# Performance work log

Hardware: AMD Instinct MI355X
Metric: run time of the kernel (lower is better)

Reference implementation:

```python
import jax, jax.numpy as jnp
import numpy as np

H = 1024      # hidden_dim == memory_dim (required by seq-axis concat)
M = 1024      # memory_dim
FF = 4096     # ff_dim
WIN = 16      # window_size
SLOTS = 10    # persistent memory slots
B, S = 2, 4096
EPS_LN = 1e-5
EPS_NORM = 1e-12


def _layernorm(x, g, b):
    m = jnp.mean(x, axis=-1, keepdims=True)
    v = jnp.var(x, axis=-1, keepdims=True)
    return (x - m) / jnp.sqrt(v + EPS_LN) * g + b


def setup_inputs() -> dict:
    key = jax.random.key(0)
    ks = jax.random.split(key, 12)

    def lin_w(k, out_d, in_d):
        return jax.random.normal(k, (out_d, in_d), jnp.float32) / np.sqrt(in_d)

    return {
        "x": jax.random.normal(ks[0], (B, S, H), jnp.float32),
        "mem_W": lin_w(ks[1], M, M), "mem_b": jnp.zeros((M,), jnp.float32),
        "P": jax.random.normal(ks[2], (SLOTS, M), jnp.float32),
        "Wi": lin_w(ks[3], M, H), "bi": jnp.zeros((M,), jnp.float32),
        "Wl1": lin_w(ks[4], M, M), "bl1": jnp.zeros((M,), jnp.float32),
        "Wl2": lin_w(ks[5], M, M), "bl2": jnp.zeros((M,), jnp.float32),
        "Wo": lin_w(ks[6], H, M), "bo": jnp.zeros((H,), jnp.float32),
        "fgate": jnp.ones((1,), jnp.float32),
        "lrate": jnp.ones((1,), jnp.float32),
        "Wg": lin_w(ks[7], H, 2 * H), "bg": jnp.zeros((H,), jnp.float32),
        "W1": lin_w(ks[8], FF, H), "b1": jnp.zeros((FF,), jnp.float32),
        "W2": lin_w(ks[9], H, FF), "b2": jnp.zeros((H,), jnp.float32),
        "g1": jnp.ones((H,), jnp.float32), "be1": jnp.zeros((H,), jnp.float32),
        "g2": jnp.ones((H,), jnp.float32), "be2": jnp.zeros((H,), jnp.float32),
        "g3": jnp.ones((H,), jnp.float32), "be3": jnp.zeros((H,), jnp.float32),
    }


def reference(x, mem_W, mem_b, P, Wi, bi, Wl1, bl1, Wl2, bl2, Wo, bo,
              fgate, lrate, Wg, bg, W1, b1, W2, b2,
              g1, be1, g2, be2, g3, be3):
    b, s, h = x.shape
    # k = concat(x, persistent) along seq; v = k.clone()
    k_full = jnp.concatenate([x, jnp.broadcast_to(P, (b,) + P.shape)], axis=1)  # [B, S+SLOTS, H]

    # sit at positions >= S and are never inside the window, so only x is attended.
    idx = jnp.arange(s)[:, None] + jnp.arange(-WIN, 1)[None, :]
    valid = idx >= 0
    k_win = k_full[:, jnp.maximum(idx, 0)]
    scores = jnp.einsum('bsh,bswh->bsw', x, k_win) * (h ** -0.5)
    scores = jnp.where(valid[None], scores, -jnp.inf)
    attn_out = jnp.einsum('bsw,bswh->bsh', jax.nn.softmax(scores, axis=-1), k_win)
    x1 = _layernorm(x + attn_out, g1, be1)

    # --- neural long-term memory (key == value since v = k.clone())
    kv = k_full.reshape(-1, h)
    kn = kv / jnp.maximum(jnp.linalg.norm(kv, axis=-1, keepdims=True), EPS_NORM)
    kp = kn @ Wi.T + bi          # projected key; value_proj is identical
    vp = kp
    hdd = jax.nn.silu(kp @ Wl1.T + bl1)
    hdd = jax.nn.silu(hdd @ Wl2.T + bl2)
    pred = hdd @ mem_W.T + mem_b
    diff = pred - vp
    n, m = diff.shape
    grad_W = (2.0 / (n * m)) * diff.T @ hdd          # d mse / d mem_W
    W_new = (1.0 - fgate) * mem_W + lrate * grad_W   # test-time memory update
    mem_out = hdd @ W_new.T + mem_b
    mo = (mem_out @ Wo.T + bo).reshape(b, -1, h)[:, :s]  # align with x seq length

    # --- gated fusion + FFN
    gate = jax.nn.sigmoid(jnp.concatenate([x1, mo], axis=-1) @ Wg.T + bg)
    combined = gate * x1 + (1.0 - gate) * mo
    x2 = _layernorm(x1 + combined, g2, be2)
    ff = jax.nn.silu(x2 @ W1.T + b1) @ W2.T + b2
    return _layernorm(x2 + ff, g3, be3)
```

## Files before the change

### kernel.cpp

```cpp
#include <hip/hip_runtime.h>
#include <hip/hip_bf16.h>

#define WIN 16
#define SLOTS 10
#define SS 4096
#define NTOK 8192
#define NKV 8212
#define NPOS 4106
#define NATTB 2048
#define NKVB 2053

typedef unsigned short u16;
typedef unsigned int u32;
typedef __attribute__((ext_vector_type(8))) short short8;
typedef __attribute__((ext_vector_type(4))) float f32x4;

__device__ __forceinline__ u16 f2bf(float f){
  union { float f; u32 u; } a; a.f = f;
  u32 r = (a.u + 0x7fff + ((a.u >> 16) & 1)) >> 16;
  return (u16)r;
}
__device__ __forceinline__ float bf2f(u16 v){
  union { u32 u; float f; } a; a.u = ((u32)v) << 16;
  return a.f;
}
__device__ __forceinline__ float wred(float v){
  #pragma unroll
  for (int off=32; off; off>>=1) v += __shfl_xor(v, off, 64);
  return v;
}

#define GLOAD(gp, lp) __builtin_amdgcn_global_load_lds( \
    (const __attribute__((address_space(1))) void*)(gp), \
    (__attribute__((address_space(3))) void*)(lp), 16, 0, 0)

#define FENCE_BARRIER() do { \
    __builtin_amdgcn_sched_barrier(0); \
    __builtin_amdgcn_s_barrier(); \
    __builtin_amdgcn_sched_barrier(0); \
  } while(0)

__global__ __launch_bounds__(256) void cvt_all(
    const float4* __restrict__ s0, const float4* __restrict__ s1,
    const float4* __restrict__ s2, const float4* __restrict__ s3,
    const float4* __restrict__ s4, const float4* __restrict__ s5,
    const float4* __restrict__ s6, const float4* __restrict__ s7,
    ushort4* __restrict__ d0, ushort4* __restrict__ d1,
    ushort4* __restrict__ d2, ushort4* __restrict__ d3,
    ushort4* __restrict__ d4, ushort4* __restrict__ d5,
    ushort4* __restrict__ d6, ushort4* __restrict__ d7)
{
  int i = blockIdx.x * 256 + threadIdx.x;
  const float4* s; ushort4* d; int base;
  if      (i <  262144){ s=s0; d=d0; base=0; }
  else if (i <  524288){ s=s1; d=d1; base=262144; }
  else if (i <  786432){ s=s2; d=d2; base=524288; }
  else if (i < 1048576){ s=s3; d=d3; base=786432; }
  else if (i < 1310720){ s=s4; d=d4; base=1048576; }
  else if (i < 1835008){ s=s5; d=d5; base=1310720; }
  else if (i < 2883584){ s=s6; d=d6; base=1835008; }
  else                 { s=s7; d=d7; base=2883584; }
  float4 v = s[i - base];
  ushort4 o; o.x=f2bf(v.x); o.y=f2bf(v.y); o.z=f2bf(v.z); o.w=f2bf(v.w);
  d[i - base] = o;
}

__global__ __launch_bounds__(256) void attn_kv(
    const float* __restrict__ x, const float* __restrict__ P,
    const float* __restrict__ g1, const float* __restrict__ be1,
    u16* __restrict__ x1b, u16* __restrict__ kn)
{
  const int blk = blockIdx.x;
  const int t = threadIdx.x, lane = t & 63, wid = t >> 6;
  if (blk >= NATTB){
    const int r = (blk - NATTB)*4 + wid;
    if (r >= NKV) return;
    const int b = r / NPOS;
    const int pos = r - b*NPOS;
    const float4* src = (const float4*)((pos < SS) ? (x + (((size_t)b*SS + pos) << 10))
                                                   : (P + ((size_t)(pos - SS) << 10)));
    float4 v[4];
    float ss = 0.f;
    #pragma unroll
    for (int e=0;e<4;e++){
      v[e] = src[(lane<<2)+e];
      ss += v[e].x*v[e].x + v[e].y*v[e].y + v[e].z*v[e].z + v[e].w*v[e].w;
    }
    ss = wred(ss);
    float inv = 1.f / fmaxf(sqrtf(ss), 1e-12f);
    ushort4* dst = (ushort4*)kn + ((size_t)r << 8);
    #pragma unroll
    for (int e=0;e<4;e++){
      ushort4 o; o.x=f2bf(v[e].x*inv); o.y=f2bf(v[e].y*inv); o.z=f2bf(v[e].z*inv); o.w=f2bf(v[e].w*inv);
      dst[(lane<<2)+e] = o;
    }
    return;
  }
  const int n = blk*4 + wid;
  const int b = n >> 12, s = n & 4095;
  const float* xb = x + ((size_t)b << 22);
  const float4* qp = (const float4*)(xb + ((size_t)s << 10));
  float4 q[4];
  #pragma unroll
  for (int e=0;e<4;e++) q[e] = qp[(lane<<2)+e];

  const int j0 = (s >= WIN) ? 0 : (WIN - s);
  float m = -3.0e38f, l = 0.f;
  float4 o[4];
  #pragma unroll
  for (int e=0;e<4;e++) o[e] = make_float4(0.f,0.f,0.f,0.f);

  for (int j = j0; j < 17; ++j){
    const float4* kp_ = (const float4*)(xb + ((size_t)(s - WIN + j) << 10));
    float4 kk[4];
    float dp = 0.f;
    #pragma unroll
    for (int e=0;e<4;e++){
      kk[e] = kp_[(lane<<2)+e];
      dp += q[e].x*kk[e].x + q[e].y*kk[e].y + q[e].z*kk[e].z + q[e].w*kk[e].w;
    }
    dp = wred(dp) * 0.03125f;
    float mn = fmaxf(m, dp);
    float sc = __expf(m - mn);
    float e_ = __expf(dp - mn);
    l = l*sc + e_;
    #pragma unroll
    for (int e=0;e<4;e++){
      o[e].x = o[e].x*sc + e_*kk[e].x;
      o[e].y = o[e].y*sc + e_*kk[e].y;
      o[e].z = o[e].z*sc + e_*kk[e].z;
      o[e].w = o[e].w*sc + e_*kk[e].w;
    }
    m = mn;
  }
  const float il = 1.f / l;
  float s1 = 0.f, s2 = 0.f;
  float4 y[4];
  #pragma unroll
  for (int e=0;e<4;e++){
    y[e].x = q[e].x + o[e].x*il;
    y[e].y = q[e].y + o[e].y*il;
    y[e].z = q[e].z + o[e].z*il;
    y[e].w = q[e].w + o[e].w*il;
    s1 += y[e].x + y[e].y + y[e].z + y[e].w;
    s2 += y[e].x*y[e].x + y[e].y*y[e].y + y[e].z*y[e].z + y[e].w*y[e].w;
  }
  s1 = wred(s1); s2 = wred(s2);
  float mean = s1 * (1.f/1024.f);
  float var  = s2 * (1.f/1024.f) - mean*mean;
  float rstd = 1.f/sqrtf(var + 1e-5f);
  ushort4* dst = (ushort4*)x1b + ((size_t)n << 8);
  #pragma unroll
  for (int e=0;e<4;e++){
    float4 gv = ((const float4*)g1)[(lane<<2)+e];
    float4 bv = ((const float4*)be1)[(lane<<2)+e];
    ushort4 ob;
    ob.x = f2bf((y[e].x-mean)*rstd*gv.x + bv.x);
    ob.y = f2bf((y[e].y-mean)*rstd*gv.y + bv.y);
    ob.z = f2bf((y[e].z-mean)*rstd*gv.z + bv.z);
    ob.w = f2bf((y[e].w-mean)*rstd*gv.w + bv.w);
    dst[(lane<<2)+e] = ob;
  }
}

template<int EPI, int SPLITA>
__global__ __launch_bounds__(256) void gemm_nt(
    const u16* __restrict__ A, const u16* __restrict__ A2,
    const u16* __restrict__ Bmat, const float* __restrict__ bias,
    const u16* __restrict__ auxb,
    float* __restrict__ Cf, u16* __restrict__ Cb,
    int N, int O, int ldA, int ldB, int klen)
{
  __shared__ __align__(16) u16 lA[4][128*32];
  __shared__ __align__(16) u16 lB[4][128*32];
  const int t = threadIdx.x;
  const int lane = t & 63;
  const int bm0 = blockIdx.x * 128;
  const int bn0 = blockIdx.y * 128;
  const int wid = t >> 6;
  const int wr = wid >> 1, wc = wid & 1;
  const int nkh = klen >> 5;

  f32x4 acc[4][4];
  #pragma unroll
  for (int i=0;i<4;i++)
    #pragma unroll
    for (int j=0;j<4;j++)
      acc[i][j] = (f32x4){0.f,0.f,0.f,0.f};

  const int srow = t >> 2;
  const int sch  = t & 3;
  const int csw  = ((sch ^ ((srow >> 1) & 3)) << 3);

  int gr0 = bm0 + srow;      gr0 = gr0 < N ? gr0 : N-1;
  int gr1 = bm0 + srow + 64; gr1 = gr1 < N ? gr1 : N-1;
  int gb0 = bn0 + srow;      gb0 = gb0 < O ? gb0 : O-1;
  int gb1 = bn0 + srow + 64; gb1 = gb1 < O ? gb1 : O-1;
  const u16* bA0 = A + (size_t)gr0*(size_t)ldA + csw;
  const u16* bA1 = A + (size_t)gr1*(size_t)ldA + csw;
  const u16* bA20 = SPLITA ? (A2 + ((size_t)gr0 << 10) + csw) : nullptr;
  const u16* bA21 = SPLITA ? (A2 + ((size_t)gr1 << 10) + csw) : nullptr;
  const u16* bB0 = Bmat + (size_t)gb0*(size_t)ldB + csw;
  const u16* bB1 = Bmat + (size_t)gb1*(size_t)ldB + csw;
  const int dLo = t << 3;
  const int dHi = (t << 3) + 2048;

  auto stage = [&](int j){
    const int kb = j << 5;
    const int s = j & 3;
    const u16* a0 = SPLITA ? ((kb < 1024) ? bA0 + kb : bA20 + (kb - 1024)) : bA0 + kb;
    const u16* a1 = SPLITA ? ((kb < 1024) ? bA1 + kb : bA21 + (kb - 1024)) : bA1 + kb;
    GLOAD(a0, &lA[s][dLo]);
    GLOAD(a1, &lA[s][dHi]);
    GLOAD(bB0 + kb, &lB[s][dLo]);
    GLOAD(bB1 + kb, &lB[s][dHi]);
  };

  stage(0);
  if (nkh > 1) stage(1);
  if (nkh > 2) stage(2);

  const int l15 = lane & 15;
  const int cq  = lane >> 4;
  const int soff = ((cq ^ ((l15 >> 1) & 3)) << 3);

  for (int j = 0; j < nkh; ++j){
    const int s = j & 3;
    const int cnt = 4*((j+1 < nkh) + (j+2 < nkh));
    if (cnt == 8)      { asm volatile("s_waitcnt vmcnt(8)" ::: "memory"); }
    else if (cnt == 4) { asm volatile("s_waitcnt vmcnt(4)" ::: "memory"); }
    else               { asm volatile("s_waitcnt vmcnt(0)" ::: "memory"); }
    FENCE_BARRIER();
    short8 af[4], bfv[4];
    #pragma unroll
    for (int mi=0;mi<4;mi++)
      af[mi] = *(const short8*)(&lA[s][((wr*64 + mi*16 + l15) * 32) + soff]);
    #pragma unroll
    for (int ni=0;ni<4;ni++)
      bfv[ni] = *(const short8*)(&lB[s][((wc*64 + ni*16 + l15) * 32) + soff]);
    if (j + 3 < nkh) stage(j + 3);
    __builtin_amdgcn_sched_barrier(0);
    __builtin_amdgcn_s_setprio(1);
    #pragma unroll
    for (int mi=0;mi<4;mi++)
      #pragma unroll
      for (int ni=0;ni<4;ni++)
        acc[mi][ni] = __builtin_amdgcn_mfma_f32_16x16x32_bf16(af[mi], bfv[ni], acc[mi][ni], 0, 0, 0);
    __builtin_amdgcn_s_setprio(0);
    __builtin_amdgcn_sched_barrier(0);
  }

  const int rbase = (lane >> 4) * 4;
  const int cidx = lane & 15;
  #pragma unroll
  for (int mi=0;mi<4;mi++){
    #pragma unroll
    for (int r=0;r<4;r++){
      const int n = bm0 + wr*64 + mi*16 + rbase + r;
      if (n >= N) continue;
      #pragma unroll
      for (int ni=0;ni<4;ni++){
        const int o = bn0 + wc*64 + ni*16 + cidx;
        float v = acc[mi][ni][r] + bias[o];
        if (EPI == 6){
          int b = n / NPOS;
          int pos = n - b*NPOS;
          if (pos < SS){
            Cb[(((size_t)(b*SS + pos)) << 10) + o] = f2bf(v);
          }
        } else {
          size_t idx = (size_t)n*(size_t)O + o;
          if (EPI == 0){ Cf[idx] = v; }
          else if (EPI == 1){ float sv = v/(1.f+__expf(-v)); Cb[idx] = f2bf(sv); }
          else if (EPI == 2){ Cb[idx] = f2bf(v); }
          else if (EPI == 4){ Cb[idx] = f2bf(v - bf2f(auxb[idx])); }
          else if (EPI == 5){ Cb[idx] = f2bf(1.f/(1.f+__expf(-v))); }
        }
      }
    }
  }
}

template<int EPI>
__global__ __launch_bounds__(512, 2) void gemm_256(
    const u16* __restrict__ A, const u16* __restrict__ Bmat,
    const float* __restrict__ bias,
    float* __restrict__ Cf, float* __restrict__ Cf2, u16* __restrict__ Cb,
    int N, int O, int ldA, int ldB, int klen)
{
  __shared__ __align__(16) u16 lA[4][256*32];
  __shared__ __align__(16) u16 lB[4][256*32];
  const int t = threadIdx.x;
  const int lane = t & 63;
  const int wid = t >> 6;
  const int wr = wid >> 2, wc = wid & 3;
  const int bm0 = blockIdx.x * 256;
  const int bn0 = blockIdx.y * 256;
  const size_t koff = (size_t)blockIdx.z * (size_t)klen;
  const int nkh = klen >> 5;

  f32x4 acc[8][4];
  #pragma unroll
  for (int i=0;i<8;i++)
    #pragma unroll
    for (int j=0;j<4;j++)
      acc[i][j] = (f32x4){0.f,0.f,0.f,0.f};

  const int srow = t >> 2;
  const int sch  = t & 3;
  const int csw  = ((sch ^ ((srow >> 1) & 3)) << 3);
  int gr0 = bm0 + srow;       gr0 = gr0 < N ? gr0 : N-1;
  int gr1 = bm0 + srow + 128; gr1 = gr1 < N ? gr1 : N-1;
  int gb0 = bn0 + srow;       gb0 = gb0 < O ? gb0 : O-1;
  int gb1 = bn0 + srow + 128; gb1 = gb1 < O ? gb1 : O-1;
  const u16* baseA0 = A    + (size_t)gr0*(size_t)ldA + koff + csw;
  const u16* baseA1 = A    + (size_t)gr1*(size_t)ldA + koff + csw;
  const u16* baseB0 = Bmat + (size_t)gb0*(size_t)ldB + koff + csw;
  const u16* baseB1 = Bmat + (size_t)gb1*(size_t)ldB + koff + csw;
  const int ldsLo = srow*32 + (sch << 3);
  const int ldsHi = (srow + 128)*32 + (sch << 3);

  auto stageA = [&](int j){
    const int kb = j << 5;
    const int s = j & 3;
    GLOAD(baseA0 + kb, &lA[s][ldsLo]);
    GLOAD(baseA1 + kb, &lA[s][ldsHi]);
  };
  auto stageB = [&](int j){
    const int kb = j << 5;
    const int s = j & 3;
    GLOAD(baseB0 + kb, &lB[s][ldsLo]);
    GLOAD(baseB1 + kb, &lB[s][ldsHi]);
  };

  stageA(0); stageB(0);
  if (nkh > 1){ stageA(1); stageB(1); }
  if (nkh > 2){ stageA(2); stageB(2); }

  const int l15 = lane & 15;
  const int cq  = lane >> 4;
  const int chS = ((cq ^ ((l15 >> 1) & 3)) << 3);

  for (int j = 0; j < nkh; ++j){
    const int s = j & 3;
    const int rem = nkh - 1 - j;
    if (rem >= 2)      { asm volatile("s_waitcnt vmcnt(8)" ::: "memory"); }
    else if (rem == 1) { asm volatile("s_waitcnt vmcnt(4)" ::: "memory"); }
    else               { asm volatile("s_waitcnt vmcnt(0)" ::: "memory"); }
    FENCE_BARRIER();
    short8 af[4], bfv[4];
    #pragma unroll
    for (int ni=0;ni<4;ni++)
      bfv[ni] = *(const short8*)(&lB[s][((wc*64 + ni*16 + l15) * 32) + chS]);
    #pragma unroll
    for (int mi=0;mi<4;mi++)
      af[mi] = *(const short8*)(&lA[s][((wr*128 + mi*16 + l15) * 32) + chS]);
    if (j + 3 < nkh) stageA(j + 3);
    __builtin_amdgcn_sched_barrier(0);
    __builtin_amdgcn_s_setprio(1);
    #pragma unroll
    for (int mi=0;mi<4;mi++)
      #pragma unroll
      for (int ni=0;ni<4;ni++)
        acc[mi][ni] = __builtin_amdgcn_mfma_f32_16x16x32_bf16(af[mi], bfv[ni], acc[mi][ni], 0, 0, 0);
    __builtin_amdgcn_s_setprio(0);
    __builtin_amdgcn_sched_barrier(0);
    FENCE_BARRIER();
    #pragma unroll
    for (int mi=0;mi<4;mi++)
      af[mi] = *(const short8*)(&lA[s][((wr*128 + (mi+4)*16 + l15) * 32) + chS]);
    if (j + 3 < nkh) stageB(j + 3);
    __builtin_amdgcn_sched_barrier(0);
    __builtin_amdgcn_s_setprio(1);
    #pragma unroll
    for (int mi=0;mi<4;mi++)
      #pragma unroll
      for (int ni=0;ni<4;ni++)
        acc[mi+4][ni] = __builtin_amdgcn_mfma_f32_16x16x32_bf16(af[mi], bfv[ni], acc[mi+4][ni], 0, 0, 0);
    __builtin_amdgcn_s_setprio(0);
    __builtin_amdgcn_sched_barrier(0);
  }

  float* dstf = (EPI == 7) ? (blockIdx.z ? Cf2 : Cf) : Cf;
  const int rbase = (lane >> 4) * 4;
  const int cidx = lane & 15;
  #pragma unroll
  for (int mi=0;mi<8;mi++){
    #pragma unroll
    for (int r=0;r<4;r++){
      const int n = bm0 + wr*128 + mi*16 + rbase + r;
      if (n >= N) continue;
      #pragma unroll
      for (int ni=0;ni<4;ni++){
        const int o = bn0 + wc*64 + ni*16 + cidx;
        size_t idx = (size_t)n*(size_t)O + o;
        if (EPI == 7){ dstf[idx] = acc[mi][ni][r]; }
        else {
          float v = acc[mi][ni][r] + bias[o];
          if (EPI == 0){ Cf[idx] = v; }
          else if (EPI == 1){ float sv = v/(1.f+__expf(-v)); Cb[idx] = f2bf(sv); }
          else if (EPI == 2){ Cb[idx] = f2bf(v); }
        }
      }
    }
  }
}

#define NSPLIT 6
__global__ __launch_bounds__(256) void gemm_tn(
    const u16* __restrict__ A, const u16* __restrict__ B,
    float* __restrict__ part0, float* __restrict__ part1)
{
  __shared__ __align__(16) u16 lA[128*64];
  __shared__ __align__(16) u16 lB[128*64];
  const int t = threadIdx.x, lane = t & 63;
  const int i0 = blockIdx.x * 128, j0 = blockIdx.y * 128, z = blockIdx.z;
  const int wid = t >> 6, wr = wid >> 1, wc = wid & 1;
  const int TILES = (NKV + 63) >> 6;
  const int PER = (TILES + NSPLIT - 1) / NSPLIT;
  const int kt0 = z * PER;
  const int ktend = (kt0 + PER < TILES) ? (kt0 + PER) : TILES;

  f32x4 acc[4][4];
  #pragma unroll
  for (int i=0;i<4;i++)
    #pragma unroll
    for (int j=0;j<4;j++)
      acc[i][j] = (f32x4){0.f,0.f,0.f,0.f};

  const int p = t & 31;
  const int g = t >> 5;

  auto loadr = [&](int kt, short8 R[8]){
    const int n0 = kt << 6;
    const int na = n0 + 2*p, nb = na + 1;
    short8 z8 = (short8){0,0,0,0,0,0,0,0};
    R[0]=z8;R[1]=z8;R[2]=z8;R[3]=z8;R[4]=z8;R[5]=z8;R[6]=z8;R[7]=z8;
    if (na < NKV){
      const u16* ra = A + (size_t)na*1024 + i0 + g*16;
      R[0] = *(const short8*)ra; R[1] = *(const short8*)(ra+8);
      const u16* rb = B + (size_t)na*1024 + j0 + g*16;
      R[4] = *(const short8*)rb; R[5] = *(const short8*)(rb+8);
    }
    if (nb < NKV){
      const u16* ra = A + (size_t)nb*1024 + i0 + g*16;
      R[2] = *(const short8*)ra; R[3] = *(const short8*)(ra+8);
      const u16* rb = B + (size_t)nb*1024 + j0 + g*16;
      R[6] = *(const short8*)rb; R[7] = *(const short8*)(rb+8);
    }
  };

  short8 cr[8], nr[8];
  loadr(kt0, cr);

  const int pc = p >> 2, pl = p & 3;

  for (int kt = kt0; kt < ktend; ++kt){
    if (kt + 1 < ktend) loadr(kt + 1, nr);
    asm volatile("" ::: "memory");
    FENCE_BARRIER();
    u32* wA = (u32*)lA; u32* wB = (u32*)lB;
    #pragma unroll
    for (int e=0;e<8;e++){
      const int s = (pc ^ e) * 4 + pl;
      wA[(g*16 + e)*32 + s]     = ((u32)(u16)cr[0][e]) | (((u32)(u16)cr[2][e]) << 16);
      wB[(g*16 + e)*32 + s]     = ((u32)(u16)cr[4][e]) | (((u32)(u16)cr[6][e]) << 16);
    }
    #pragma unroll
    for (int e=0;e<8;e++){
      const int s = (pc ^ e) * 4 + pl;
      wA[(g*16 + 8 + e)*32 + s] = ((u32)(u16)cr[1][e]) | (((u32)(u16)cr[3][e]) << 16);
      wB[(g*16 + 8 + e)*32 + s] = ((u32)(u16)cr[5][e]) | (((u32)(u16)cr[7][e]) << 16);
    }
    asm volatile("s_waitcnt lgkmcnt(0)" ::: "memory");
    FENCE_BARRIER();
    const int l15 = lane & 15;
    const int rx = l15 & 7;
    const int cq = lane >> 4;
    #pragma unroll
    for (int kk=0;kk<2;kk++){
      const int soff = (((kk*4 + cq) ^ rx) << 3);
      short8 af[4], bfv[4];
      #pragma unroll
      for (int mi=0;mi<4;mi++)
        af[mi] = *(const short8*)(lA + ((wr*64 + mi*16 + l15) << 6) + soff);
      #pragma unroll
      for (int ni=0;ni<4;ni++)
        bfv[ni] = *(const short8*)(lB + ((wc*64 + ni*16 + l15) << 6) + soff);
      #pragma unroll
      for (int mi=0;mi<4;mi++)
        #pragma unroll
        for (int ni=0;ni<4;ni++)
          acc[mi][ni] = __builtin_amdgcn_mfma_f32_16x16x32_bf16(af[mi], bfv[ni], acc[mi][ni], 0, 0, 0);
    }
    #pragma unroll
    for (int e=0;e<8;e++) cr[e] = nr[e];
  }

  float* dst = (z < 4) ? (part0 + ((size_t)z << 20)) : (part1 + ((size_t)(z-4) << 20));
  const int rbase = (lane >> 4) * 4;
  const int cidx = lane & 15;
  #pragma unroll
  for (int mi=0;mi<4;mi++)
    #pragma unroll
    for (int r=0;r<4;r++){
      const int i = i0 + wr*64 + mi*16 + rbase + r;
      #pragma unroll
      for (int ni=0;ni<4;ni++){
        const int j = j0 + wc*64 + ni*16 + cidx;
        dst[((size_t)i << 10) + j] = acc[mi][ni][r];
      }
    }
}

__global__ __launch_bounds__(256) void wnew_k(const float* __restrict__ part0,
                                              const float* __restrict__ part1,
                                              const float* __restrict__ memW,
                                              const float* __restrict__ fg,
                                              const float* __restrict__ lr,
                                              u16* __restrict__ out)
{
  int i = blockIdx.x*256 + threadIdx.x;
  float s = part0[i] + part0[i + (1<<20)] + part0[i + (2<<20)] + part0[i + (3<<20)]
          + part1[i] + part1[i + (1<<20)];
  const float scale = 2.f / ((float)NKV * 1024.f);
  float v = (1.f - fg[0])*memW[i] + lr[0]*scale*s;
  out[i] = f2bf(v);
}

__global__ __launch_bounds__(256) void ln_gate(
    const u16* __restrict__ x1b, const u16* __restrict__ gateb,
    const u16* __restrict__ mob, const float* __restrict__ g2,
    const float* __restrict__ be2, u16* __restrict__ x2b)
{
  const int n = blockIdx.x;
  const int t = threadIdx.x, lane = t & 63, w = t >> 6;
  const size_t rb = (size_t)n << 8;
  ushort4 xa = ((const ushort4*)x1b)[rb+t];
  ushort4 ga = ((const ushort4*)gateb)[rb+t];
  ushort4 ma = ((const ushort4*)mob)[rb+t];
  float a0=bf2f(xa.x),a1=bf2f(xa.y),a2=bf2f(xa.z),a3=bf2f(xa.w);
  float g0=bf2f(ga.x),g1v=bf2f(ga.y),g2v=bf2f(ga.z),g3v=bf2f(ga.w);
  float m0=bf2f(ma.x),m1=bf2f(ma.y),m2=bf2f(ma.z),m3=bf2f(ma.w);
  float y0 = a0 + g0*a0 + (1.f-g0)*m0;
  float y1 = a1 + g1v*a1 + (1.f-g1v)*m1;
  float y2 = a2 + g2v*a2 + (1.f-g2v)*m2;
  float y3 = a3 + g3v*a3 + (1.f-g3v)*m3;
  float s1 = y0+y1+y2+y3;
  float s2 = y0*y0+y1*y1+y2*y2+y3*y3;
  #pragma unroll
  for (int off=32; off; off>>=1){ s1 += __shfl_xor(s1, off, 64); s2 += __shfl_xor(s2, off, 64); }
  __shared__ float rsh[8];
  if (lane == 0){ rsh[w] = s1; rsh[4+w] = s2; }
  __syncthreads();
  float S1 = rsh[0]+rsh[1]+rsh[2]+rsh[3];
  float S2 = rsh[4]+rsh[5]+rsh[6]+rsh[7];
  float mean = S1 * (1.f/1024.f);
  float var  = S2 * (1.f/1024.f) - mean*mean;
  float rstd = 1.f/sqrtf(var + 1e-5f);
  float4 gv = ((const float4*)g2)[t];
  float4 bv = ((const float4*)be2)[t];
  ushort4 ob;
  ob.x = f2bf((y0-mean)*rstd*gv.x + bv.x);
  ob.y = f2bf((y1-mean)*rstd*gv.y + bv.y);
  ob.z = f2bf((y2-mean)*rstd*gv.z + bv.z);
  ob.w = f2bf((y3-mean)*rstd*gv.w + bv.w);
  ((ushort4*)x2b)[rb + t] = ob;
}

__global__ __launch_bounds__(256) void ln_final(
    const u16* __restrict__ x2b, const float* __restrict__ g3,
    const float* __restrict__ be3, float* __restrict__ out)
{
  const int n = blockIdx.x;
  const int t = threadIdx.x, lane = t & 63, w = t >> 6;
  const size_t rb = (size_t)n << 8;
  ushort4 xa = ((const ushort4*)x2b)[rb+t];
  float4 f = ((const float4*)out)[rb+t];
  float y0 = bf2f(xa.x)+f.x, y1 = bf2f(xa.y)+f.y, y2 = bf2f(xa.z)+f.z, y3 = bf2f(xa.w)+f.w;
  float s1 = y0+y1+y2+y3;
  float s2 = y0*y0+y1*y1+y2*y2+y3*y3;
  #pragma unroll
  for (int off=32; off; off>>=1){ s1 += __shfl_xor(s1, off, 64); s2 += __shfl_xor(s2, off, 64); }
  __shared__ float rsh[8];
  if (lane == 0){ rsh[w] = s1; rsh[4+w] = s2; }
  __syncthreads();
  float S1 = rsh[0]+rsh[1]+rsh[2]+rsh[3];
  float S2 = rsh[4]+rsh[5]+rsh[6]+rsh[7];
  float mean = S1 * (1.f/1024.f);
  float var  = S2 * (1.f/1024.f) - mean*mean;
  float rstd = 1.f/sqrtf(var + 1e-5f);
  float4 gv = ((const float4*)g3)[t];
  float4 bv = ((const float4*)be3)[t];
  float4 o;
  o.x = (y0-mean)*rstd*gv.x + bv.x;
  o.y = (y1-mean)*rstd*gv.y + bv.y;
  o.z = (y2-mean)*rstd*gv.z + bv.z;
  o.w = (y3-mean)*rstd*gv.w + bv.w;
  ((float4*)out)[rb + t] = o;
}

__global__ __launch_bounds__(256) void ln_final2(
    const u16* __restrict__ x2b, const float* __restrict__ p0,
    const float* __restrict__ p1, const float* __restrict__ b2,
    const float* __restrict__ g3, const float* __restrict__ be3,
    float* __restrict__ out)
{
  const int n = blockIdx.x;
  const int t = threadIdx.x, lane = t & 63, w = t >> 6;
  const size_t rb = (size_t)n << 8;
  ushort4 xa = ((const ushort4*)x2b)[rb+t];
  float4 f0 = ((const float4*)p0)[rb+t];
  float4 f1 = ((const float4*)p1)[rb+t];
  float4 bb = ((const float4*)b2)[t];
  float y0 = bf2f(xa.x)+f0.x+f1.x+bb.x, y1 = bf2f(xa.y)+f0.y+f1.y+bb.y;
  float y2 = bf2f(xa.z)+f0.z+f1.z+bb.z, y3 = bf2f(xa.w)+f0.w+f1.w+bb.w;
  float s1 = y0+y1+y2+y3;
  float s2 = y0*y0+y1*y1+y2*y2+y3*y3;
  #pragma unroll
  for (int off=32; off; off>>=1){ s1 += __shfl_xor(s1, off, 64); s2 += __shfl_xor(s2, off, 64); }
  __shared__ float rsh[8];
  if (lane == 0){ rsh[w] = s1; rsh[4+w] = s2; }
  __syncthreads();
  float S1 = rsh[0]+rsh[1]+rsh[2]+rsh[3];
  float S2 = rsh[4]+rsh[5]+rsh[6]+rsh[7];
  float mean = S1 * (1.f/1024.f);
  float var  = S2 * (1.f/1024.f) - mean*mean;
  float rstd = 1.f/sqrtf(var + 1e-5f);
  float4 gv = ((const float4*)g3)[t];
  float4 bv = ((const float4*)be3)[t];
  float4 o;
  o.x = (y0-mean)*rstd*gv.x + bv.x;
  o.y = (y1-mean)*rstd*gv.y + bv.y;
  o.z = (y2-mean)*rstd*gv.z + bv.z;
  o.w = (y3-mean)*rstd*gv.w + bv.w;
  ((float4*)out)[rb + t] = o;
}

extern "C" void kernel_launch(void* const* d_in, const int* in_sizes, int n_in,
                              void* d_out, int out_size, void* d_ws, size_t ws_size,
                              hipStream_t stream)
{
  const float* x    = (const float*)d_in[0];
  const float* memW = (const float*)d_in[1];
  const float* memb = (const float*)d_in[2];
  const float* P    = (const float*)d_in[3];
  const float* Wi   = (const float*)d_in[4];
  const float* bi   = (const float*)d_in[5];
  const float* Wl1  = (const float*)d_in[6];
  const float* bl1  = (const float*)d_in[7];
  const float* Wl2  = (const float*)d_in[8];
  const float* bl2  = (const float*)d_in[9];
  const float* Wo   = (const float*)d_in[10];
  const float* bo   = (const float*)d_in[11];
  const float* fg   = (const float*)d_in[12];
  const float* lr   = (const float*)d_in[13];
  const float* Wg   = (const float*)d_in[14];
  const float* bg   = (const float*)d_in[15];
  const float* W1   = (const float*)d_in[16];
  const float* b1   = (const float*)d_in[17];
  const float* W2   = (const float*)d_in[18];
  const float* b2   = (const float*)d_in[19];
  const float* g1   = (const float*)d_in[20];
  const float* be1  = (const float*)d_in[21];
  const float* g2   = (const float*)d_in[22];
  const float* be2  = (const float*)d_in[23];
  const float* g3   = (const float*)d_in[24];
  const float* be3  = (const float*)d_in[25];
  float* out = (float*)d_out;

  const size_t SZ_TOK = (size_t)NTOK*1024*2;
  const size_t SZ_KV  = (size_t)NKV*1024*2;
  char* base = (char*)d_ws;
  size_t off = 0;
  auto alloc = [&](size_t bytes) -> char* {
    char* p = base + off;
    off += (bytes + 255) & ~(size_t)255;
    return p;
  };
  u16* x1b   = (u16*)alloc(SZ_TOK);
  u16* knb   = (u16*)alloc(SZ_KV);
  u16* h1b   = (u16*)alloc(SZ_KV);
  u16* hddb  = (u16*)alloc(SZ_KV);
  u16* kpb   = (u16*)alloc(SZ_KV);
  u16* wnewb = (u16*)alloc((size_t)1024*1024*2);
  u16* WiB   = (u16*)alloc((size_t)1024*1024*2);
  u16* Wl1B  = (u16*)alloc((size_t)1024*1024*2);
  u16* Wl2B  = (u16*)alloc((size_t)1024*1024*2);
  u16* memWB = (u16*)alloc((size_t)1024*1024*2);
  u16* WoB   = (u16*)alloc((size_t)1024*1024*2);
  u16* WgB   = (u16*)alloc((size_t)1024*2048*2);
  u16* W1B   = (u16*)alloc((size_t)4096*1024*2);
  u16* W2B   = (u16*)alloc((size_t)1024*4096*2);
  const size_t off_base = off;
  if (ws_size < off_base) return;

  float* ffp0 = (float*)alloc((size_t)NTOK*1024*4);
  float* ffp1 = (float*)alloc((size_t)NTOK*1024*4);
  const bool use_split_ff2 = (ws_size >= off);

  u16*   diffb   = knb;
  float* part0   = (float*)kpb;
  float* part1   = (float*)WiB;
  u16*   memoutb = knb;
  u16*   mob     = h1b;
  u16*   gateb   = hddb;
  u16*   x2b     = kpb;
  u16*   ff1b    = x1b;

  cvt_all<<<15360, 256, 0, stream>>>(
      (const float4*)Wi, (const float4*)Wl1, (const float4*)Wl2, (const float4*)memW,
      (const float4*)Wo, (const float4*)Wg, (const float4*)W1, (const float4*)W2,
      (ushort4*)WiB, (ushort4*)Wl1B, (ushort4*)Wl2B, (ushort4*)memWB,
      (ushort4*)WoB, (ushort4*)WgB, (ushort4*)W1B, (ushort4*)W2B);

  attn_kv<<<NATTB + NKVB, 256, 0, stream>>>(x, P, g1, be1, x1b, knb);

  dim3 gkv(65, 8, 1);
  gemm_nt<2,0><<<gkv, 256, 0, stream>>>(knb, nullptr, WiB, bi, nullptr, nullptr, kpb, NKV, 1024, 1024, 1024, 1024);
  gemm_nt<1,0><<<gkv, 256, 0, stream>>>(kpb, nullptr, Wl1B, bl1, nullptr, nullptr, h1b, NKV, 1024, 1024, 1024, 1024);
  gemm_nt<1,0><<<gkv, 256, 0, stream>>>(h1b, nullptr, Wl2B, bl2, nullptr, nullptr, hddb, NKV, 1024, 1024, 1024, 1024);
  gemm_nt<4,0><<<gkv, 256, 0, stream>>>(hddb, nullptr, memWB, memb, kpb, nullptr, diffb, NKV, 1024, 1024, 1024, 1024);
  gemm_tn<<<dim3(8, 8, NSPLIT), 256, 0, stream>>>(diffb, hddb, part0, part1);
  wnew_k<<<4096, 256, 0, stream>>>(part0, part1, memW, fg, lr, wnewb);
  gemm_nt<2,0><<<gkv, 256, 0, stream>>>(hddb, nullptr, wnewb, memb, nullptr, nullptr, memoutb, NKV, 1024, 1024, 1024, 1024);
  gemm_nt<6,0><<<gkv, 256, 0, stream>>>(memoutb, nullptr, WoB, bo, nullptr, nullptr, mob, NKV, 1024, 1024, 1024, 1024);
  gemm_nt<5,1><<<dim3(64, 8, 1), 256, 0, stream>>>(x1b, mob, WgB, bg, nullptr, nullptr, gateb, NTOK, 1024, 1024, 2048, 2048);
  ln_gate<<<NTOK, 256, 0, stream>>>(x1b, gateb, mob, g2, be2, x2b);
  gemm_256<1><<<dim3(32, 16, 1), 512, 0, stream>>>(x2b, W1B, b1, nullptr, nullptr, ff1b, NTOK, 4096, 1024, 1024, 1024);
  if (use_split_ff2){
    gemm_256<7><<<dim3(32, 4, 2), 512, 0, stream>>>(ff1b, W2B, nullptr, ffp0, ffp1, nullptr, NTOK, 1024, 4096, 4096, 2048);
    ln_final2<<<NTOK, 256, 0, stream>>>(x2b, ffp0, ffp1, b2, g3, be3, out);
  } else {
    gemm_nt<0,0><<<dim3(64, 8, 1), 256, 0, stream>>>(ff1b, nullptr, W2B, b2, nullptr, out, nullptr, NTOK, 1024, 4096, 4096, 4096);
    ln_final<<<NTOK, 256, 0, stream>>>(x2b, g3, be3, out);
  }
}
```

Measured before the change: 607.9 us.

## Rework 256-tile GEMM to BK=64 double buffer, drop split-K FF2, grid-stride cvt

The 256x256 GEMM now stages 64-wide K tiles into two LDS buffers instead of four 32-wide buffers, with an 8-chunk XOR swizzle and both K sub-steps issued per barrier pair. The split-K FF2 path and its ln_final2 kernel are removed, so FF2 runs on the smaller gemm_nt tile kernel followed by ln_final. The weight conversion kernel becomes a grid-stride loop over 2048 blocks. The aim is fewer barriers per K element and less workspace, but FF2 loses the large-tile kernel and the two-way K split, and prefetch depth drops from three stages to two.

```diff
diff --git a/kernel.cpp b/kernel.cpp
--- a/kernel.cpp
+++ b/kernel.cpp
@@ -9,6 +9,7 @@
 #define NPOS 4106
 #define NATTB 2048
 #define NKVB 2053
+#define CVT_N 3932160
 
 typedef unsigned short u16;
 typedef unsigned int u32;
@@ -50,19 +51,20 @@
     ushort4* __restrict__ d4, ushort4* __restrict__ d5,
     ushort4* __restrict__ d6, ushort4* __restrict__ d7)
 {
-  int i = blockIdx.x * 256 + threadIdx.x;
-  const float4* s; ushort4* d; int base;
-  if      (i <  262144){ s=s0; d=d0; base=0; }
-  else if (i <  524288){ s=s1; d=d1; base=262144; }
-  else if (i <  786432){ s=s2; d=d2; base=524288; }
-  else if (i < 1048576){ s=s3; d=d3; base=786432; }
-  else if (i < 1310720){ s=s4; d=d4; base=1048576; }
-  else if (i < 1835008){ s=s5; d=d5; base=1310720; }
-  else if (i < 2883584){ s=s6; d=d6; base=1835008; }
-  else                 { s=s7; d=d7; base=2883584; }
-  float4 v = s[i - base];
-  ushort4 o; o.x=f2bf(v.x); o.y=f2bf(v.y); o.z=f2bf(v.z); o.w=f2bf(v.w);
-  d[i - base] = o;
+  for (int i = blockIdx.x * 256 + threadIdx.x; i < CVT_N; i += 2048*256){
+    const float4* s; ushort4* d; int base;
+    if      (i <  262144){ s=s0; d=d0; base=0; }
+    else if (i <  524288){ s=s1; d=d1; base=262144; }
+    else if (i <  786432){ s=s2; d=d2; base=524288; }
+    else if (i < 1048576){ s=s3; d=d3; base=786432; }
+    else if (i < 1310720){ s=s4; d=d4; base=1048576; }
+    else if (i < 1835008){ s=s5; d=d5; base=1310720; }
+    else if (i < 2883584){ s=s6; d=d6; base=1835008; }
+    else                 { s=s7; d=d7; base=2883584; }
+    float4 v = s[i - base];
+    ushort4 o; o.x=f2bf(v.x); o.y=f2bf(v.y); o.z=f2bf(v.z); o.w=f2bf(v.w);
+    d[i - base] = o;
+  }
 }
 
 __global__ __launch_bounds__(256) void attn_kv(
@@ -285,19 +287,18 @@
 __global__ __launch_bounds__(512, 2) void gemm_256(
     const u16* __restrict__ A, const u16* __restrict__ Bmat,
     const float* __restrict__ bias,
-    float* __restrict__ Cf, float* __restrict__ Cf2, u16* __restrict__ Cb,
+    float* __restrict__ Cf, u16* __restrict__ Cb,
     int N, int O, int ldA, int ldB, int klen)
 {
-  __shared__ __align__(16) u16 lA[4][256*32];
-  __shared__ __align__(16) u16 lB[4][256*32];
+  __shared__ __align__(16) u16 lA[2][256*64];
+  __shared__ __align__(16) u16 lB[2][256*64];
   const int t = threadIdx.x;
   const int lane = t & 63;
   const int wid = t >> 6;
   const int wr = wid >> 2, wc = wid & 3;
   const int bm0 = blockIdx.x * 256;
   const int bn0 = blockIdx.y * 256;
-  const size_t koff = (size_t)blockIdx.z * (size_t)klen;
-  const int nkh = klen >> 5;
+  const int nkt = klen >> 6;
 
   f32x4 acc[8][4];
   #pragma unroll
@@ -306,82 +307,65 @@
     for (int j=0;j<4;j++)
       acc[i][j] = (f32x4){0.f,0.f,0.f,0.f};
 
-  const int srow = t >> 2;
-  const int sch  = t & 3;
-  const int csw  = ((sch ^ ((srow >> 1) & 3)) << 3);
-  int gr0 = bm0 + srow;       gr0 = gr0 < N ? gr0 : N-1;
-  int gr1 = bm0 + srow + 128; gr1 = gr1 < N ? gr1 : N-1;
-  int gb0 = bn0 + srow;       gb0 = gb0 < O ? gb0 : O-1;
-  int gb1 = bn0 + srow + 128; gb1 = gb1 < O ? gb1 : O-1;
-  const u16* baseA0 = A    + (size_t)gr0*(size_t)ldA + koff + csw;
-  const u16* baseA1 = A    + (size_t)gr1*(size_t)ldA + koff + csw;
-  const u16* baseB0 = Bmat + (size_t)gb0*(size_t)ldB + koff + csw;
-  const u16* baseB1 = Bmat + (size_t)gb1*(size_t)ldB + koff + csw;
-  const int ldsLo = srow*32 + (sch << 3);
-  const int ldsHi = (srow + 128)*32 + (sch << 3);
-
-  auto stageA = [&](int j){
-    const int kb = j << 5;
-    const int s = j & 3;
-    GLOAD(baseA0 + kb, &lA[s][ldsLo]);
-    GLOAD(baseA1 + kb, &lA[s][ldsHi]);
+  const int srow = t >> 3;
+  const int sch  = t & 7;
+  const int csw  = ((sch ^ (srow & 7)) << 3);
+  const u16* baseA[4]; const u16* baseB[4];
+  #pragma unroll
+  for (int i=0;i<4;i++){
+    int gr = bm0 + srow + i*64; gr = gr < N ? gr : N-1;
+    baseA[i] = A + (size_t)gr*(size_t)ldA + csw;
+    int gb = bn0 + srow + i*64; gb = gb < O ? gb : O-1;
+    baseB[i] = Bmat + (size_t)gb*(size_t)ldB + csw;
+  }
+  const int dbase = srow*64 + (sch << 3);
+
+  auto stage = [&](int j){
+    const int kb = j << 6;
+    const int s = j & 1;
+    #pragma unroll
+    for (int i=0;i<4;i++){
+      GLOAD(baseA[i] + kb, &lA[s][dbase + i*4096]);
+      GLOAD(baseB[i] + kb, &lB[s][dbase + i*4096]);
+    }
   };
-  auto stageB = [&](int j){
-    const int kb = j << 5;
-    const int s = j & 3;
-    GLOAD(baseB0 + kb, &lB[s][ldsLo]);
-    GLOAD(baseB1 + kb, &lB[s][ldsHi]);
-  };
-
-  stageA(0); stageB(0);
-  if (nkh > 1){ stageA(1); stageB(1); }
-  if (nkh > 2){ stageA(2); stageB(2); }
+
+  stage(0);
+  if (nkt > 1) stage(1);
 
   const int l15 = lane & 15;
   const int cq  = lane >> 4;
-  const int chS = ((cq ^ ((l15 >> 1) & 3)) << 3);
-
-  for (int j = 0; j < nkh; ++j){
-    const int s = j & 3;
-    const int rem = nkh - 1 - j;
-    if (rem >= 2)      { asm volatile("s_waitcnt vmcnt(8)" ::: "memory"); }
-    else if (rem == 1) { asm volatile("s_waitcnt vmcnt(4)" ::: "memory"); }
-    else               { asm volatile("s_waitcnt vmcnt(0)" ::: "memory"); }
+  const int rx  = l15 & 7;
+
+  for (int j = 0; j < nkt; ++j){
+    const int s = j & 1;
+    if (j + 1 < nkt) { asm volatile("s_waitcnt vmcnt(8)" ::: "memory"); }
+    else             { asm volatile("s_waitcnt vmcnt(0)" ::: "memory"); }
     FENCE_BARRIER();
-    short8 af[4], bfv[4];
-    #pragma unroll
-    for (int ni=0;ni<4;ni++)
-      bfv[ni] = *(const short8*)(&lB[s][((wc*64 + ni*16 + l15) * 32) + chS]);
-    #pragma unroll
-    for (int mi=0;mi<4;mi++)
-      af[mi] = *(const short8*)(&lA[s][((wr*128 + mi*16 + l15) * 32) + chS]);
-    if (j + 3 < nkh) stageA(j + 3);
-    __builtin_amdgcn_sched_barrier(0);
-    __builtin_amdgcn_s_setprio(1);
-    #pragma unroll
-    for (int mi=0;mi<4;mi++)
+    #pragma unroll
+    for (int kk=0; kk<2; kk++){
+      const int soff = (((kk*4 + cq) ^ rx) << 3);
+      short8 af[8], bfv[4];
       #pragma unroll
       for (int ni=0;ni<4;ni++)
-        acc[mi][ni] = __builtin_amdgcn_mfma_f32_16x16x32_bf16(af[mi], bfv[ni], acc[mi][ni], 0, 0, 0);
-    __builtin_amdgcn_s_setprio(0);
-    __builtin_amdgcn_sched_barrier(0);
+        bfv[ni] = *(const short8*)(&lB[s][((wc*64 + ni*16 + l15) << 6) + soff]);
+      #pragma unroll
+      for (int mi=0;mi<8;mi++)
+        af[mi] = *(const short8*)(&lA[s][((wr*128 + mi*16 + l15) << 6) + soff]);
+      __builtin_amdgcn_sched_barrier(0);
+      __builtin_amdgcn_s_setprio(1);
+      #pragma unroll
+      for (int mi=0;mi<8;mi++)
+        #pragma unroll
+        for (int ni=0;ni<4;ni++)
+          acc[mi][ni] = __builtin_amdgcn_mfma_f32_16x16x32_bf16(af[mi], bfv[ni], acc[mi][ni], 0, 0, 0);
+      __builtin_amdgcn_s_setprio(0);
+      __builtin_amdgcn_sched_barrier(0);
+    }
     FENCE_BARRIER();
-    #pragma unroll
-    for (int mi=0;mi<4;mi++)
-      af[mi] = *(const short8*)(&lA[s][((wr*128 + (mi+4)*16 + l15) * 32) + chS]);
-    if (j + 3 < nkh) stageB(j + 3);
-    __builtin_amdgcn_sched_barrier(0);
-    __builtin_amdgcn_s_setprio(1);
-    #pragma unroll
-    for (int mi=0;mi<4;mi++)
-      #pragma unroll
-      for (int ni=0;ni<4;ni++)
-        acc[mi+4][ni] = __builtin_amdgcn_mfma_f32_16x16x32_bf16(af[mi], bfv[ni], acc[mi+4][ni], 0, 0, 0);
-    __builtin_amdgcn_s_setprio(0);
-    __builtin_amdgcn_sched_barrier(0);
-  }
-
-  float* dstf = (EPI == 7) ? (blockIdx.z ? Cf2 : Cf) : Cf;
+    if (j + 2 < nkt) stage(j + 2);
+  }
+
   const int rbase = (lane >> 4) * 4;
   const int cidx = lane & 15;
   #pragma unroll
@@ -393,14 +377,11 @@
       #pragma unroll
       for (int ni=0;ni<4;ni++){
         const int o = bn0 + wc*64 + ni*16 + cidx;
+        float v = acc[mi][ni][r] + bias[o];
         size_t idx = (size_t)n*(size_t)O + o;
-        if (EPI == 7){ dstf[idx] = acc[mi][ni][r]; }
-        else {
-          float v = acc[mi][ni][r] + bias[o];
-          if (EPI == 0){ Cf[idx] = v; }
-          else if (EPI == 1){ float sv = v/(1.f+__expf(-v)); Cb[idx] = f2bf(sv); }
-          else if (EPI == 2){ Cb[idx] = f2bf(v); }
-        }
+        if (EPI == 0){ Cf[idx] = v; }
+        else if (EPI == 1){ float sv = v/(1.f+__expf(-v)); Cb[idx] = f2bf(sv); }
+        else if (EPI == 2){ Cb[idx] = f2bf(v); }
       }
     }
   }
@@ -578,43 +559,6 @@
   ushort4 xa = ((const ushort4*)x2b)[rb+t];
   float4 f = ((const float4*)out)[rb+t];
   float y0 = bf2f(xa.x)+f.x, y1 = bf2f(xa.y)+f.y, y2 = bf2f(xa.z)+f.z, y3 = bf2f(xa.w)+f.w;
-  float s1 = y0+y1+y2+y3;
-  float s2 = y0*y0+y1*y1+y2*y2+y3*y3;
-  #pragma unroll
-  for (int off=32; off; off>>=1){ s1 += __shfl_xor(s1, off, 64); s2 += __shfl_xor(s2, off, 64); }
-  __shared__ float rsh[8];
-  if (lane == 0){ rsh[w] = s1; rsh[4+w] = s2; }
-  __syncthreads();
-  float S1 = rsh[0]+rsh[1]+rsh[2]+rsh[3];
-  float S2 = rsh[4]+rsh[5]+rsh[6]+rsh[7];
-  float mean = S1 * (1.f/1024.f);
-  float var  = S2 * (1.f/1024.f) - mean*mean;
-  float rstd = 1.f/sqrtf(var + 1e-5f);
-  float4 gv = ((const float4*)g3)[t];
-  float4 bv = ((const float4*)be3)[t];
-  float4 o;
-  o.x = (y0-mean)*rstd*gv.x + bv.x;
-  o.y = (y1-mean)*rstd*gv.y + bv.y;
-  o.z = (y2-mean)*rstd*gv.z + bv.z;
-  o.w = (y3-mean)*rstd*gv.w + bv.w;
-  ((float4*)out)[rb + t] = o;
-}
-
-__global__ __launch_bounds__(256) void ln_final2(
-    const u16* __restrict__ x2b, const float* __restrict__ p0,
-    const float* __restrict__ p1, const float* __restrict__ b2,
-    const float* __restrict__ g3, const float* __restrict__ be3,
-    float* __restrict__ out)
-{
-  const int n = blockIdx.x;
-  const int t = threadIdx.x, lane = t & 63, w = t >> 6;
-  const size_t rb = (size_t)n << 8;
-  ushort4 xa = ((const ushort4*)x2b)[rb+t];
-  float4 f0 = ((const float4*)p0)[rb+t];
-  float4 f1 = ((const float4*)p1)[rb+t];
-  float4 bb = ((const float4*)b2)[t];
-  float y0 = bf2f(xa.x)+f0.x+f1.x+bb.x, y1 = bf2f(xa.y)+f0.y+f1.y+bb.y;
-  float y2 = bf2f(xa.z)+f0.z+f1.z+bb.z, y3 = bf2f(xa.w)+f0.w+f1.w+bb.w;
   float s1 = y0+y1+y2+y3;
   float s2 = y0*y0+y1*y1+y2*y2+y3*y3;
   #pragma unroll
@@ -692,12 +636,7 @@
   u16* WgB   = (u16*)alloc((size_t)1024*2048*2);
   u16* W1B   = (u16*)alloc((size_t)4096*1024*2);
   u16* W2B   = (u16*)alloc((size_t)1024*4096*2);
-  const size_t off_base = off;
-  if (ws_size < off_base) return;
-
-  float* ffp0 = (float*)alloc((size_t)NTOK*1024*4);
-  float* ffp1 = (float*)alloc((size_t)NTOK*1024*4);
-  const bool use_split_ff2 = (ws_size >= off);
+  if (ws_size < off) return;
 
   u16*   diffb   = knb;
   float* part0   = (float*)kpb;
@@ -708,7 +647,7 @@
   u16*   x2b     = kpb;
   u16*   ff1b    = x1b;
 
-  cvt_all<<<15360, 256, 0, stream>>>(
+  cvt_all<<<2048, 256, 0, stream>>>(
       (const float4*)Wi, (const float4*)Wl1, (const float4*)Wl2, (const float4*)memW,
       (const float4*)Wo, (const float4*)Wg, (const float4*)W1, (const float4*)W2,
       (ushort4*)WiB, (ushort4*)Wl1B, (ushort4*)Wl2B, (ushort4*)memWB,
@@ -727,12 +666,7 @@
   gemm_nt<6,0><<<gkv, 256, 0, stream>>>(memoutb, nullptr, WoB, bo, nullptr, nullptr, mob, NKV, 1024, 1024, 1024, 1024);
   gemm_nt<5,1><<<dim3(64, 8, 1), 256, 0, stream>>>(x1b, mob, WgB, bg, nullptr, nullptr, gateb, NTOK, 1024, 1024, 2048, 2048);
   ln_gate<<<NTOK, 256, 0, stream>>>(x1b, gateb, mob, g2, be2, x2b);
-  gemm_256<1><<<dim3(32, 16, 1), 512, 0, stream>>>(x2b, W1B, b1, nullptr, nullptr, ff1b, NTOK, 4096, 1024, 1024, 1024);
-  if (use_split_ff2){
-    gemm_256<7><<<dim3(32, 4, 2), 512, 0, stream>>>(ff1b, W2B, nullptr, ffp0, ffp1, nullptr, NTOK, 1024, 4096, 4096, 2048);
-    ln_final2<<<NTOK, 256, 0, stream>>>(x2b, ffp0, ffp1, b2, g3, be3, out);
-  } else {
-    gemm_nt<0,0><<<dim3(64, 8, 1), 256, 0, stream>>>(ff1b, nullptr, W2B, b2, nullptr, out, nullptr, NTOK, 1024, 4096, 4096, 4096);
-    ln_final<<<NTOK, 256, 0, stream>>>(x2b, g3, be3, out);
-  }
-}
+  gemm_256<1><<<dim3(32, 16, 1), 512, 0, stream>>>(x2b, W1B, b1, nullptr, ff1b, NTOK, 4096, 1024, 1024, 1024);
+  gemm_nt<0,0><<<dim3(64, 8, 1), 256, 0, stream>>>(ff1b, nullptr, W2B, b2, nullptr, out, nullptr, NTOK, 1024, 4096, 4096, 4096);
+  ln_final<<<NTOK, 256, 0, stream>>>(x2b, g3, be3, out);
+}
```

After: 608.0 us. No clear change (+0.0%).
